# Performance work log

Measured on AMD Instinct MI355X. Metric: run time of the kernel, lower is better.

## Reference

```python
import jax, jax.numpy as jnp
import numpy as np

D_MODEL = 1024
N_HEAD = 16
D_FF = 4 * D_MODEL
LN_EPS = 1e-5


def _layernorm(x, g, b):
    mu = jnp.mean(x, axis=-1, keepdims=True)
    var = jnp.mean(jnp.square(x - mu), axis=-1, keepdims=True)
    return (x - mu) * jax.lax.rsqrt(var + LN_EPS) * g + b


def _mha(q_in, k_in, v_in, mask, wq, bq, wk, wv, bv, wo, bo):
    B, Tq, D = q_in.shape
    H, Dk = N_HEAD, D // N_HEAD
    q = (q_in @ wq + bq).reshape(B, Tq, H, Dk).transpose(0, 2, 1, 3)      # [B,H,Tq,Dk]
    k = (k_in @ wk).reshape(B, -1, H, Dk).transpose(0, 2, 1, 3)           # [B,H,Tk,Dk]
    v = (v_in @ wv + bv).reshape(B, -1, H, Dk).transpose(0, 2, 1, 3)      # [B,H,Tk,Dk]
    attn = jnp.einsum('bhqd,bhkd->bhqk', q, k) / jnp.sqrt(jnp.float32(Dk))
    if mask is not None:
        m0 = (mask[:, None, :, :] == 0)                                    # [B,1,Tq,Tk]
        attn = jnp.where(m0, -jnp.inf, attn)
        attn = jax.nn.softmax(attn, axis=-1)
        attn = jnp.where(m0, 0.0, attn)
    else:
        attn = jax.nn.softmax(attn, axis=-1)
    out = jnp.einsum('bhqk,bhkd->bhqd', attn, v)
    out = out.transpose(0, 2, 1, 3).reshape(B, Tq, D)
    return out @ wo + bo


def setup_inputs() -> dict:
    key = jax.random.key(0)
    ks = jax.random.split(key, 32)
    B, T, S, D = 4, 1024, 1024, D_MODEL
    w = lambda k, shp: 0.02 * jax.random.normal(k, shp, dtype=jnp.float32)
    inp = {
        'dec_input': jax.random.normal(ks[0], (B, T, D), dtype=jnp.float32),
        'enc_output': jax.random.normal(ks[1], (B, S, D), dtype=jnp.float32),
        'self_mask': jnp.broadcast_to(jnp.tril(jnp.ones((T, T), jnp.int32)), (B, T, T)),
        'cross_mask': jnp.ones((B, T, S), jnp.int32),
        'sa_ln_g': jnp.ones((D,), jnp.float32), 'sa_ln_b': jnp.zeros((D,), jnp.float32),
        'sa_wq': w(ks[2], (D, D)), 'sa_bq': jnp.zeros((D,), jnp.float32),
        'sa_wk': w(ks[3], (D, D)),
        'sa_wv': w(ks[4], (D, D)), 'sa_bv': jnp.zeros((D,), jnp.float32),
        'sa_wo': w(ks[5], (D, D)), 'sa_bo': jnp.zeros((D,), jnp.float32),
        'ca_ln_g': jnp.ones((D,), jnp.float32), 'ca_ln_b': jnp.zeros((D,), jnp.float32),
        'ca_wq': w(ks[6], (D, D)), 'ca_bq': jnp.zeros((D,), jnp.float32),
        'ca_wk': w(ks[7], (D, D)),
        'ca_wv': w(ks[8], (D, D)), 'ca_bv': jnp.zeros((D,), jnp.float32),
        'ca_wo': w(ks[9], (D, D)), 'ca_bo': jnp.zeros((D,), jnp.float32),
        'mlp_ln_g': jnp.ones((D,), jnp.float32), 'mlp_ln_b': jnp.zeros((D,), jnp.float32),
        'w1': w(ks[10], (D, D_FF)), 'b1': jnp.zeros((D_FF,), jnp.float32),
        'w2': w(ks[11], (D_FF, D)), 'b2': jnp.zeros((D,), jnp.float32),
    }
    return inp


def reference(dec_input, enc_output, self_mask, cross_mask,
              sa_ln_g, sa_ln_b, sa_wq, sa_bq, sa_wk, sa_wv, sa_bv, sa_wo, sa_bo,
              ca_ln_g, ca_ln_b, ca_wq, ca_bq, ca_wk, ca_wv, ca_bv, ca_wo, ca_bo,
              mlp_ln_g, mlp_ln_b, w1, b1, w2, b2):
    # self-attention block (pre-norm, residual)
    x = _layernorm(dec_input, sa_ln_g, sa_ln_b)
    x = dec_input + _mha(x, x, x, self_mask, sa_wq, sa_bq, sa_wk, sa_wv, sa_bv, sa_wo, sa_bo)
    # cross-attention block
    h = _layernorm(x, ca_ln_g, ca_ln_b)
    x = x + _mha(h, enc_output, enc_output, cross_mask, ca_wq, ca_bq, ca_wk, ca_wv, ca_bv, ca_wo, ca_bo)
    # GELU FFN block
    h = _layernorm(x, mlp_ln_g, mlp_ln_b)
    x = x + (jax.nn.gelu(h @ w1 + b1, approximate=False) @ w2 + b2)
    return x
```

## Files before the change

kernel.cpp:

```cpp
#include <hip/hip_runtime.h>
#include <math.h>

typedef unsigned short u16;
typedef unsigned int   u32;
typedef __attribute__((ext_vector_type(8))) short bf16x8;
typedef __attribute__((ext_vector_type(4))) float f32x4;

__device__ __forceinline__ u16 f2bf(float f) {
  u32 u = __builtin_bit_cast(u32, f);
  u += 0x7fffu + ((u >> 16) & 1u);
  return (u16)(u >> 16);
}
__device__ __forceinline__ u32 cvtpk(float lo, float hi_) {
  u32 r;
  asm("v_cvt_pk_bf16_f32 %0, %1, %2" : "=v"(r) : "v"(lo), "v"(hi_));
  return r;
}

__device__ __forceinline__ void g2l16(const u16* g, u16* l) {
  __builtin_amdgcn_global_load_lds(
      (const __attribute__((address_space(1))) unsigned int*)g,
      (__attribute__((address_space(3))) unsigned int*)l, 16, 0, 0);
}

struct TC8 { const float* s[8]; u16* d[8]; };
__global__ __launch_bounds__(256)
void transcvt8_kernel(TC8 p) {
  const float* __restrict__ W = p.s[blockIdx.z];
  u16* __restrict__ Wt = p.d[blockIdx.z];
  __shared__ float tile[32][33];
  const int n0 = blockIdx.x * 32, k0 = blockIdx.y * 32;
  const int tx = threadIdx.x & 31, ty = threadIdx.x >> 5;
  for (int i = 0; i < 4; ++i)
    tile[ty + 8 * i][tx] = W[(size_t)(k0 + ty + 8 * i) * 1024 + n0 + tx];
  __syncthreads();
  for (int i = 0; i < 4; ++i)
    Wt[(size_t)(n0 + ty + 8 * i) * 1024 + k0 + tx] = f2bf(tile[tx][ty + 8 * i]);
}

__global__ __launch_bounds__(256)
void transcvt_kernel(const float* __restrict__ W, u16* __restrict__ Wt, int K, int N) {
  __shared__ float tile[32][33];
  const int n0 = blockIdx.x * 32, k0 = blockIdx.y * 32;
  const int tx = threadIdx.x & 31, ty = threadIdx.x >> 5;
  for (int i = 0; i < 4; ++i)
    tile[ty + 8 * i][tx] = W[(size_t)(k0 + ty + 8 * i) * N + n0 + tx];
  __syncthreads();
  for (int i = 0; i < 4; ++i)
    Wt[(size_t)(n0 + ty + 8 * i) * K + k0 + tx] = f2bf(tile[tx][ty + 8 * i]);
}

__global__ __launch_bounds__(256)
void cvt_kernel(const float* __restrict__ in, u16* __restrict__ out) {
  const int i = blockIdx.x * 256 + threadIdx.x;
  const float4 v = ((const float4*)in)[i];
  u16 o[4] = {f2bf(v.x), f2bf(v.y), f2bf(v.z), f2bf(v.w)};
  ((ushort4*)out)[i] = *(ushort4*)o;
}

__global__ __launch_bounds__(256)
void pack_bias_kernel(const float* __restrict__ bq, const float* __restrict__ bv,
                      const float* __restrict__ cbv,
                      float* __restrict__ B3, float* __restrict__ B2) {
  const int i = blockIdx.x * 256 + threadIdx.x;
  if (i < 3072) {
    float v = 0.0f;
    if (i < 1024) v = bq[i];
    else if (i >= 2048) v = bv[i - 2048];
    B3[i] = v;
  } else {
    const int j = i - 3072;
    B2[j] = (j >= 1024) ? cbv[j - 1024] : 0.0f;
  }
}

__global__ __launch_bounds__(256)
void ln_kernel(const float* __restrict__ x, const float* __restrict__ g,
               const float* __restrict__ b, u16* __restrict__ out) {
  const int row = blockIdx.x;
  const float4 v4 = ((const float4*)(x + (size_t)row * 1024))[threadIdx.x];
  float vv[4] = {v4.x, v4.y, v4.z, v4.w};
  float s = vv[0] + vv[1] + vv[2] + vv[3];
  float s2 = vv[0] * vv[0] + vv[1] * vv[1] + vv[2] * vv[2] + vv[3] * vv[3];
  for (int m = 1; m < 64; m <<= 1) { s += __shfl_xor(s, m); s2 += __shfl_xor(s2, m); }
  __shared__ float ss[4], ss2[4];
  const int w = threadIdx.x >> 6;
  if ((threadIdx.x & 63) == 0) { ss[w] = s; ss2[w] = s2; }
  __syncthreads();
  s = ss[0] + ss[1] + ss[2] + ss[3];
  s2 = ss2[0] + ss2[1] + ss2[2] + ss2[3];
  const float mu = s * (1.0f / 1024.0f);
  const float var = s2 * (1.0f / 1024.0f) - mu * mu;
  const float r = rsqrtf(var + 1e-5f);
  const int c = threadIdx.x * 4;
  const float4 g4 = ((const float4*)g)[threadIdx.x];
  const float4 b4 = ((const float4*)b)[threadIdx.x];
  float gg[4] = {g4.x, g4.y, g4.z, g4.w};
  float bb[4] = {b4.x, b4.y, b4.z, b4.w};
  u16 o[4];
  for (int j = 0; j < 4; ++j) o[j] = f2bf((vv[j] - mu) * r * gg[j] + bb[j]);
  ((ushort4*)(out + (size_t)row * 1024 + c))[0] = *(ushort4*)o;
}

template<bool RES_F32, bool GELU>
__global__ __launch_bounds__(512)
void gemm_kernel(const u16* __restrict__ A, const u16* __restrict__ Bt,
                 const float* __restrict__ bias, const float* __restrict__ res,
                 void* __restrict__ Cout, int M, int N, int K) {
  __shared__ u16 As[2][128][32];
  __shared__ u16 Bs[2][128][32];
  const int t = threadIdx.x, lane = t & 63, w = t >> 6;
  const int wr = w >> 2, wc = w & 3;
  const int nwg = gridDim.x * gridDim.y;
  int bid = blockIdx.y * gridDim.x + blockIdx.x;
  bid = (bid & 7) * (nwg >> 3) + (bid >> 3);
  const int m0 = (bid / gridDim.x) * 128, n0 = (bid % gridDim.x) * 128;
  const int fr = lane & 15, fg = lane >> 4;
  const int srow = lane >> 2, scol = (lane & 3) * 8;
  const u16* Ag = &A[(size_t)(m0 + w * 16 + srow) * K + scol];
  const u16* Bg = &Bt[(size_t)(n0 + w * 16 + srow) * K + scol];
  f32x4 acc[4][2] = {};
  g2l16(Ag, &As[0][w * 16][0]);
  g2l16(Bg, &Bs[0][w * 16][0]);
  __syncthreads();
  int cur = 0;
  for (int k0 = 0; k0 < K; k0 += 32) {
    if (k0 + 32 < K) {
      const int nx = cur ^ 1, kn = k0 + 32;
      g2l16(Ag + kn, &As[nx][w * 16][0]);
      g2l16(Bg + kn, &Bs[nx][w * 16][0]);
    }
    bf16x8 af[4], bfr[2];
    for (int m = 0; m < 4; ++m) af[m] = *(bf16x8*)&As[cur][wr * 64 + m * 16 + fr][fg * 8];
    for (int n = 0; n < 2; ++n) bfr[n] = *(bf16x8*)&Bs[cur][wc * 32 + n * 16 + fr][fg * 8];
    __builtin_amdgcn_s_setprio(1);
    for (int m = 0; m < 4; ++m)
      for (int n = 0; n < 2; ++n)
        acc[m][n] = __builtin_amdgcn_mfma_f32_16x16x32_bf16(af[m], bfr[n], acc[m][n], 0, 0, 0);
    __builtin_amdgcn_s_setprio(0);
    __syncthreads();
    cur ^= 1;
  }
  for (int m = 0; m < 4; ++m)
    for (int n = 0; n < 2; ++n) {
      const int col = n0 + wc * 32 + n * 16 + fr;
      const float bv = bias ? bias[col] : 0.0f;
      for (int i = 0; i < 4; ++i) {
        const int row = m0 + wr * 64 + m * 16 + fg * 4 + i;
        float v = acc[m][n][i] + bv;
        if (GELU) v = 0.5f * v * (1.0f + erff(v * 0.70710678118654752f));
        if (RES_F32)
          ((float*)Cout)[(size_t)row * N + col] = res[(size_t)row * N + col] + v;
        else
          ((u16*)Cout)[(size_t)row * N + col] = f2bf(v);
      }
    }
}

template<bool CAUSAL>
__global__ __launch_bounds__(512)
void attn_kernel(const u16* __restrict__ Q, int ldq,
                 const u16* __restrict__ K, int ldk,
                 const u16* __restrict__ V, int ldv,
                 u16* __restrict__ O) {
  __shared__ u16 VsT[2][64][64];
  __shared__ u16 Ps[8][16][72];
  const int bh = blockIdx.x, b = bh >> 4, h = bh & 15;
  const int qy = blockIdx.y;
  const int t = threadIdx.x, w = t >> 6, lane = t & 63;
  const int ql = lane & 15;
  const int hi = lane >> 4;
  const int qr = qy * 128 + w * 16;
  const int qz = qr + ql;
  const int hcol = h * 64;
  const int nkt = CAUSAL ? 2 * qy + 2 : 16;
  const int wlim = CAUSAL ? (qr >> 6) : nkt - 1;
  const u16* Kb = K + (size_t)(b * 1024) * ldk + hcol;
  const u16* Vb = V + (size_t)(b * 1024) * ldv + hcol;
  const size_t qgrow = (size_t)(b * 1024 + qz) * ldq + hcol;
  const bf16x8 qb0 = *(const bf16x8*)&Q[qgrow + hi * 8];
  const bf16x8 qb1 = *(const bf16x8*)&Q[qgrow + 32 + hi * 8];
  f32x4 o[4] = {};
  float mrow = -1e30f, lsum = 0.0f;
  const int sp = t >> 3, sm = t & 7;
  const float c1 = 0.125f * 1.44269504f;
  if (t < 256) {
    const bf16x8 va = *(const bf16x8*)&Vb[(size_t)(2 * sp) * ldv + 8 * sm];
    const bf16x8 vb = *(const bf16x8*)&Vb[(size_t)(2 * sp + 1) * ldv + 8 * sm];
    #pragma unroll
    for (int jj = 0; jj < 8; ++jj) {
      u32 pr = (u32)((const u16*)&va)[jj] | ((u32)((const u16*)&vb)[jj] << 16);
      *(u32*)&VsT[0][8 * sm + jj][(2 * sp) ^ ((jj ^ sm) << 3)] = pr;
    }
  }
  bf16x8 kA[8], kB[8];
  #pragma unroll
  for (int j = 0; j < 4; ++j) {
    kA[j]     = *(const bf16x8*)&Kb[(size_t)(j * 16 + ql) * ldk + hi * 8];
    kA[4 + j] = *(const bf16x8*)&Kb[(size_t)(j * 16 + ql) * ldk + 32 + hi * 8];
  }
  __syncthreads();

  auto body = [&](bf16x8 (&kc)[8], bf16x8 (&kn)[8], const int kt) {
    const int k0 = kt * 64;
    bf16x8 va, vb;
    const bool stageV = (kt + 1 < nkt) && (t < 256);
    if (stageV) {
      va = *(const bf16x8*)&Vb[(size_t)(k0 + 64 + 2 * sp) * ldv + 8 * sm];
      vb = *(const bf16x8*)&Vb[(size_t)(k0 + 64 + 2 * sp + 1) * ldv + 8 * sm];
    }
    if (kt + 1 <= wlim) {
      #pragma unroll
      for (int j = 0; j < 4; ++j) {
        kn[j]     = *(const bf16x8*)&Kb[(size_t)(k0 + 64 + j * 16 + ql) * ldk + hi * 8];
        kn[4 + j] = *(const bf16x8*)&Kb[(size_t)(k0 + 64 + j * 16 + ql) * ldk + 32 + hi * 8];
      }
    }
    if (kt <= wlim) {
      f32x4 s[4] = {};
      __builtin_amdgcn_s_setprio(1);
      #pragma unroll
      for (int j = 0; j < 4; ++j)
        s[j] = __builtin_amdgcn_mfma_f32_16x16x32_bf16(kc[j], qb0, s[j], 0, 0, 0);
      #pragma unroll
      for (int j = 0; j < 4; ++j)
        s[j] = __builtin_amdgcn_mfma_f32_16x16x32_bf16(kc[4 + j], qb1, s[j], 0, 0, 0);
      __builtin_amdgcn_s_setprio(0);
      float e2[4][4];
      float rm = -1e30f;
      const bool domask = CAUSAL && (kt == wlim);
      #pragma unroll
      for (int j = 0; j < 4; ++j)
        #pragma unroll
        for (int i = 0; i < 4; ++i) {
          float a = s[j][i] * c1;
          if (domask && (k0 + j * 16 + hi * 4 + i > qz)) a = -1e30f;
          e2[j][i] = a;
          rm = fmaxf(rm, a);
        }
      if (!__all(rm <= mrow + 8.0f)) {
        rm = fmaxf(rm, __shfl_xor(rm, 16));
        rm = fmaxf(rm, __shfl_xor(rm, 32));
        const float mn = fmaxf(mrow, rm);
        const float sc = exp2f(mrow - mn);
        lsum *= sc;
        float scv[4];
        #pragma unroll
        for (int i = 0; i < 4; ++i) scv[i] = __shfl(sc, hi * 4 + i);
        #pragma unroll
        for (int nb = 0; nb < 4; ++nb)
          #pragma unroll
          for (int i = 0; i < 4; ++i) o[nb][i] *= scv[i];
        mrow = mn;
      }
      float p[4][4];
      #pragma unroll
      for (int j = 0; j < 4; ++j)
        #pragma unroll
        for (int i = 0; i < 4; ++i) { p[j][i] = exp2f(e2[j][i] - mrow); lsum += p[j][i]; }
      #pragma unroll
      for (int j = 0; j < 4; ++j) {
        *(u32*)&Ps[w][ql][j * 16 + hi * 4]     = cvtpk(p[j][0], p[j][1]);
        *(u32*)&Ps[w][ql][j * 16 + hi * 4 + 2] = cvtpk(p[j][2], p[j][3]);
      }
      asm volatile("s_waitcnt lgkmcnt(0)" ::: "memory");
      __builtin_amdgcn_sched_barrier(0);
      const bf16x8 pa0 = *(const bf16x8*)&Ps[w][ql][hi * 8];
      const bf16x8 pa1 = *(const bf16x8*)&Ps[w][ql][32 + hi * 8];
      __builtin_amdgcn_s_setprio(1);
      #pragma unroll
      for (int nb = 0; nb < 4; ++nb) {
        const int dim = nb * 16 + ql;
        const int swz = ((dim & 7) ^ ((dim >> 3) & 7)) << 3;
        const bf16x8 v0 = *(const bf16x8*)&VsT[kt & 1][dim][(hi * 8) ^ swz];
        const bf16x8 v1 = *(const bf16x8*)&VsT[kt & 1][dim][(32 + hi * 8) ^ swz];
        o[nb] = __builtin_amdgcn_mfma_f32_16x16x32_bf16(pa0, v0, o[nb], 0, 0, 0);
        o[nb] = __builtin_amdgcn_mfma_f32_16x16x32_bf16(pa1, v1, o[nb], 0, 0, 0);
      }
      __builtin_amdgcn_s_setprio(0);
    }
    if (stageV) {
      const int nx = (kt & 1) ^ 1;
      #pragma unroll
      for (int jj = 0; jj < 8; ++jj) {
        u32 pr = (u32)((const u16*)&va)[jj] | ((u32)((const u16*)&vb)[jj] << 16);
        *(u32*)&VsT[nx][8 * sm + jj][(2 * sp) ^ ((jj ^ sm) << 3)] = pr;
      }
    }
    __syncthreads();
  };

  for (int kt = 0; kt < nkt; kt += 2) {
    body(kA, kB, kt);
    if (kt + 1 < nkt) body(kB, kA, kt + 1);
  }

  float ltot = lsum + __shfl_xor(lsum, 16);
  ltot += __shfl_xor(ltot, 32);
  const float inv = 1.0f / ltot;
  #pragma unroll
  for (int i = 0; i < 4; ++i) {
    const float invq = __shfl(inv, hi * 4 + i);
    const size_t row = (size_t)(b * 1024 + qr + hi * 4 + i);
    #pragma unroll
    for (int nb = 0; nb < 4; ++nb)
      O[row * 1024 + hcol + nb * 16 + ql] = f2bf(o[nb][i] * invq);
  }
}

extern "C" void kernel_launch(void* const* d_in, const int* in_sizes, int n_in,
                              void* d_out, int out_size, void* d_ws, size_t ws_size,
                              hipStream_t stream) {
  const float* dec  = (const float*)d_in[0];
  const float* enc  = (const float*)d_in[1];
  const float* sa_g = (const float*)d_in[4];
  const float* sa_b = (const float*)d_in[5];
  const float* sa_wq = (const float*)d_in[6];
  const float* sa_bq = (const float*)d_in[7];
  const float* sa_wk = (const float*)d_in[8];
  const float* sa_wv = (const float*)d_in[9];
  const float* sa_bv = (const float*)d_in[10];
  const float* sa_wo = (const float*)d_in[11];
  const float* sa_bo = (const float*)d_in[12];
  const float* ca_g = (const float*)d_in[13];
  const float* ca_b = (const float*)d_in[14];
  const float* ca_wq = (const float*)d_in[15];
  const float* ca_bq = (const float*)d_in[16];
  const float* ca_wk = (const float*)d_in[17];
  const float* ca_wv = (const float*)d_in[18];
  const float* ca_bv = (const float*)d_in[19];
  const float* ca_wo = (const float*)d_in[20];
  const float* ca_bo = (const float*)d_in[21];
  const float* mlp_g = (const float*)d_in[22];
  const float* mlp_b = (const float*)d_in[23];
  const float* w1 = (const float*)d_in[24];
  const float* b1 = (const float*)d_in[25];
  const float* w2 = (const float*)d_in[26];
  const float* b2 = (const float*)d_in[27];

  const size_t MB = 1024 * 1024;
  if (ws_size < 97 * MB) return;
  char* ws = (char*)d_ws;
  u16* WQKV = (u16*)(ws + 0 * MB);
  u16* CQT  = (u16*)(ws + 6 * MB);
  u16* CKV  = (u16*)(ws + 8 * MB);
  u16* WOT  = (u16*)(ws + 12 * MB);
  u16* COT  = (u16*)(ws + 14 * MB);
  float* B3 = (float*)(ws + 16 * MB);
  float* B2 = (float*)(ws + 16 * MB + 16384);
  u16* XLN  = (u16*)(ws + 17 * MB);
  u16* AO   = (u16*)(ws + 25 * MB);
  u16* W1T  = (u16*)(ws + 25 * MB);
  u16* ENC  = (u16*)(ws + 33 * MB);
  u16* FB   = (u16*)(ws + 41 * MB);
  u16* EF   = (u16*)(ws + 41 * MB);
  u16* CQB  = (u16*)(ws + 57 * MB);
  u16* H1   = (u16*)(ws + 33 * MB);
  float* X1 = (float*)(ws + 65 * MB);
  u16* W2T  = (u16*)(ws + 65 * MB);
  float* X2 = (float*)(ws + 81 * MB);
  float* OUT = (float*)d_out;

  const dim3 blk(256), gblk(512), ablk(512);
  TC8 tc;
  tc.s[0] = sa_wq; tc.d[0] = WQKV;
  tc.s[1] = sa_wk; tc.d[1] = WQKV + 1024 * 1024;
  tc.s[2] = sa_wv; tc.d[2] = WQKV + 2048 * 1024;
  tc.s[3] = sa_wo; tc.d[3] = WOT;
  tc.s[4] = ca_wq; tc.d[4] = CQT;
  tc.s[5] = ca_wk; tc.d[5] = CKV;
  tc.s[6] = ca_wv; tc.d[6] = CKV + 1024 * 1024;
  tc.s[7] = ca_wo; tc.d[7] = COT;
  transcvt8_kernel<<<dim3(32, 32, 8), blk, 0, stream>>>(tc);
  pack_bias_kernel<<<dim3(20), blk, 0, stream>>>(sa_bq, sa_bv, ca_bv, B3, B2);
  cvt_kernel<<<dim3(4096), blk, 0, stream>>>(enc, ENC);

  ln_kernel<<<dim3(4096), blk, 0, stream>>>(dec, sa_g, sa_b, XLN);
  gemm_kernel<false, false><<<dim3(24, 32), gblk, 0, stream>>>(XLN, WQKV, B3, nullptr, FB, 4096, 3072, 1024);
  attn_kernel<true><<<dim3(64, 8), ablk, 0, stream>>>(FB, 3072, FB + 1024, 3072, FB + 2048, 3072, AO);
  gemm_kernel<true, false><<<dim3(8, 32), gblk, 0, stream>>>(AO, WOT, sa_bo, dec, X1, 4096, 1024, 1024);

  ln_kernel<<<dim3(4096), blk, 0, stream>>>(X1, ca_g, ca_b, XLN);
  gemm_kernel<false, false><<<dim3(16, 32), gblk, 0, stream>>>(ENC, CKV, B2, nullptr, EF, 4096, 2048, 1024);
  gemm_kernel<false, false><<<dim3(8, 32), gblk, 0, stream>>>(XLN, CQT, ca_bq, nullptr, CQB, 4096, 1024, 1024);
  attn_kernel<false><<<dim3(64, 8), ablk, 0, stream>>>(CQB, 1024, EF, 2048, EF + 1024, 2048, AO);
  gemm_kernel<true, false><<<dim3(8, 32), gblk, 0, stream>>>(AO, COT, ca_bo, X1, X2, 4096, 1024, 1024);

  transcvt_kernel<<<dim3(128, 32), blk, 0, stream>>>(w1, W1T, 1024, 4096);
  transcvt_kernel<<<dim3(32, 128), blk, 0, stream>>>(w2, W2T, 4096, 1024);
  ln_kernel<<<dim3(4096), blk, 0, stream>>>(X2, mlp_g, mlp_b, XLN);
  gemm_kernel<false, true><<<dim3(32, 32), gblk, 0, stream>>>(XLN, W1T, b1, nullptr, H1, 4096, 4096, 1024);
  gemm_kernel<true, false><<<dim3(8, 32), gblk, 0, stream>>>(H1, W2T, b2, X2, OUT, 4096, 1024, 4096);
}
```

Measured before the change: 451.5 us.

## Pre-transpose V in a separate kernel and keep attention P in registers

Adds a vtrans kernel that writes V as a per-head transposed buffer, so attention reads V fragments directly from global memory instead of staging them through a swizzled LDS double buffer. The P matrix is rearranged into MFMA operand layout with cross-lane shuffles instead of a round trip through shared memory. This removes all LDS use and __syncthreads from the attention loop. Attention blocks shrink to 256 threads covering 64 query rows, doubling the grid. The trade is two extra kernel launches, an extra V write and read through global memory, and more shuffle instructions per tile.

```diff
diff --git a/kernel.cpp b/kernel.cpp
--- a/kernel.cpp
+++ b/kernel.cpp
@@ -5,6 +5,7 @@
 typedef unsigned int   u32;
 typedef __attribute__((ext_vector_type(8))) short bf16x8;
 typedef __attribute__((ext_vector_type(4))) float f32x4;
+typedef __attribute__((ext_vector_type(4))) u32 u32x4;
 
 __device__ __forceinline__ u16 f2bf(float f) {
   u32 u = __builtin_bit_cast(u32, f);
@@ -48,6 +49,25 @@
   __syncthreads();
   for (int i = 0; i < 4; ++i)
     Wt[(size_t)(n0 + ty + 8 * i) * K + k0 + tx] = f2bf(tile[tx][ty + 8 * i]);
+}
+
+__global__ __launch_bounds__(256)
+void vtrans_kernel(const u16* __restrict__ V, int ldv, u16* __restrict__ VT) {
+  __shared__ u16 tile[64][72];
+  const int bh = blockIdx.y, b = bh >> 4, h = bh & 15;
+  const int k0 = blockIdx.x * 64;
+  const int t = threadIdx.x;
+  const int r = t >> 2, c16 = (t & 3) * 16;
+  const u16* src = &V[(size_t)(b * 1024 + k0 + r) * ldv + h * 64 + c16];
+  *(bf16x8*)&tile[r][c16] = *(const bf16x8*)&src[0];
+  *(bf16x8*)&tile[r][c16 + 8] = *(const bf16x8*)&src[8];
+  __syncthreads();
+  u16 tmp[16];
+  #pragma unroll
+  for (int j = 0; j < 16; ++j) tmp[j] = tile[c16 + j][r];
+  u16* dst = &VT[((size_t)bh << 16) + (size_t)r * 1024 + k0 + c16];
+  *(bf16x8*)&dst[0] = *(bf16x8*)&tmp[0];
+  *(bf16x8*)&dst[8] = *(bf16x8*)&tmp[8];
 }
 
 __global__ __launch_bounds__(256)
@@ -158,136 +178,128 @@
 }
 
 template<bool CAUSAL>
-__global__ __launch_bounds__(512)
+__global__ __launch_bounds__(256)
 void attn_kernel(const u16* __restrict__ Q, int ldq,
                  const u16* __restrict__ K, int ldk,
-                 const u16* __restrict__ V, int ldv,
+                 const u16* __restrict__ VT,
                  u16* __restrict__ O) {
-  __shared__ u16 VsT[2][64][64];
-  __shared__ u16 Ps[8][16][72];
   const int bh = blockIdx.x, b = bh >> 4, h = bh & 15;
   const int qy = blockIdx.y;
   const int t = threadIdx.x, w = t >> 6, lane = t & 63;
   const int ql = lane & 15;
   const int hi = lane >> 4;
-  const int qr = qy * 128 + w * 16;
+  const int qr = qy * 64 + w * 16;
   const int qz = qr + ql;
   const int hcol = h * 64;
-  const int nkt = CAUSAL ? 2 * qy + 2 : 16;
-  const int wlim = CAUSAL ? (qr >> 6) : nkt - 1;
+  const int nkt = CAUSAL ? qy + 1 : 16;
   const u16* Kb = K + (size_t)(b * 1024) * ldk + hcol;
-  const u16* Vb = V + (size_t)(b * 1024) * ldv + hcol;
+  const u16* Vb = VT + ((size_t)bh << 16);
   const size_t qgrow = (size_t)(b * 1024 + qz) * ldq + hcol;
   const bf16x8 qb0 = *(const bf16x8*)&Q[qgrow + hi * 8];
   const bf16x8 qb1 = *(const bf16x8*)&Q[qgrow + 32 + hi * 8];
   f32x4 o[4] = {};
   float mrow = -1e30f, lsum = 0.0f;
-  const int sp = t >> 3, sm = t & 7;
   const float c1 = 0.125f * 1.44269504f;
-  if (t < 256) {
-    const bf16x8 va = *(const bf16x8*)&Vb[(size_t)(2 * sp) * ldv + 8 * sm];
-    const bf16x8 vb = *(const bf16x8*)&Vb[(size_t)(2 * sp + 1) * ldv + 8 * sm];
-    #pragma unroll
-    for (int jj = 0; jj < 8; ++jj) {
-      u32 pr = (u32)((const u16*)&va)[jj] | ((u32)((const u16*)&vb)[jj] << 16);
-      *(u32*)&VsT[0][8 * sm + jj][(2 * sp) ^ ((jj ^ sm) << 3)] = pr;
-    }
-  }
+  const bool odd = (lane & 16) != 0;
+
   bf16x8 kA[8], kB[8];
   #pragma unroll
   for (int j = 0; j < 4; ++j) {
     kA[j]     = *(const bf16x8*)&Kb[(size_t)(j * 16 + ql) * ldk + hi * 8];
     kA[4 + j] = *(const bf16x8*)&Kb[(size_t)(j * 16 + ql) * ldk + 32 + hi * 8];
   }
-  __syncthreads();
 
   auto body = [&](bf16x8 (&kc)[8], bf16x8 (&kn)[8], const int kt) {
     const int k0 = kt * 64;
-    bf16x8 va, vb;
-    const bool stageV = (kt + 1 < nkt) && (t < 256);
-    if (stageV) {
-      va = *(const bf16x8*)&Vb[(size_t)(k0 + 64 + 2 * sp) * ldv + 8 * sm];
-      vb = *(const bf16x8*)&Vb[(size_t)(k0 + 64 + 2 * sp + 1) * ldv + 8 * sm];
-    }
-    if (kt + 1 <= wlim) {
+    bf16x8 vf[4][2];
+    #pragma unroll
+    for (int nb = 0; nb < 4; ++nb) {
+      const u16* vrow = &Vb[(size_t)(nb * 16 + ql) * 1024 + k0];
+      vf[nb][0] = *(const bf16x8*)&vrow[hi * 8];
+      vf[nb][1] = *(const bf16x8*)&vrow[32 + hi * 8];
+    }
+    if (kt + 1 < nkt) {
       #pragma unroll
       for (int j = 0; j < 4; ++j) {
         kn[j]     = *(const bf16x8*)&Kb[(size_t)(k0 + 64 + j * 16 + ql) * ldk + hi * 8];
         kn[4 + j] = *(const bf16x8*)&Kb[(size_t)(k0 + 64 + j * 16 + ql) * ldk + 32 + hi * 8];
       }
     }
-    if (kt <= wlim) {
-      f32x4 s[4] = {};
-      __builtin_amdgcn_s_setprio(1);
+    f32x4 s[4] = {};
+    __builtin_amdgcn_s_setprio(1);
+    #pragma unroll
+    for (int j = 0; j < 4; ++j)
+      s[j] = __builtin_amdgcn_mfma_f32_16x16x32_bf16(kc[j], qb0, s[j], 0, 0, 0);
+    #pragma unroll
+    for (int j = 0; j < 4; ++j)
+      s[j] = __builtin_amdgcn_mfma_f32_16x16x32_bf16(kc[4 + j], qb1, s[j], 0, 0, 0);
+    __builtin_amdgcn_s_setprio(0);
+    float e2[4][4];
+    float rm = -1e30f;
+    const bool domask = CAUSAL && (kt == nkt - 1);
+    #pragma unroll
+    for (int j = 0; j < 4; ++j)
       #pragma unroll
-      for (int j = 0; j < 4; ++j)
-        s[j] = __builtin_amdgcn_mfma_f32_16x16x32_bf16(kc[j], qb0, s[j], 0, 0, 0);
+      for (int i = 0; i < 4; ++i) {
+        float a = s[j][i] * c1;
+        if (domask && (k0 + j * 16 + hi * 4 + i > qz)) a = -1e30f;
+        e2[j][i] = a;
+        rm = fmaxf(rm, a);
+      }
+    if (!__all(rm <= mrow + 8.0f)) {
+      rm = fmaxf(rm, __shfl_xor(rm, 16));
+      rm = fmaxf(rm, __shfl_xor(rm, 32));
+      const float mn = fmaxf(mrow, rm);
+      const float sc = exp2f(mrow - mn);
+      lsum *= sc;
+      float scv[4];
       #pragma unroll
-      for (int j = 0; j < 4; ++j)
-        s[j] = __builtin_amdgcn_mfma_f32_16x16x32_bf16(kc[4 + j], qb1, s[j], 0, 0, 0);
-      __builtin_amdgcn_s_setprio(0);
-      float e2[4][4];
-      float rm = -1e30f;
-      const bool domask = CAUSAL && (kt == wlim);
+      for (int i = 0; i < 4; ++i) scv[i] = __shfl(sc, hi * 4 + i);
       #pragma unroll
-      for (int j = 0; j < 4; ++j)
+      for (int nb = 0; nb < 4; ++nb)
         #pragma unroll
-        for (int i = 0; i < 4; ++i) {
-          float a = s[j][i] * c1;
-          if (domask && (k0 + j * 16 + hi * 4 + i > qz)) a = -1e30f;
-          e2[j][i] = a;
-          rm = fmaxf(rm, a);
-        }
-      if (!__all(rm <= mrow + 8.0f)) {
-        rm = fmaxf(rm, __shfl_xor(rm, 16));
-        rm = fmaxf(rm, __shfl_xor(rm, 32));
-        const float mn = fmaxf(mrow, rm);
-        const float sc = exp2f(mrow - mn);
-        lsum *= sc;
-        float scv[4];
-        #pragma unroll
-        for (int i = 0; i < 4; ++i) scv[i] = __shfl(sc, hi * 4 + i);
-        #pragma unroll
-        for (int nb = 0; nb < 4; ++nb)
-          #pragma unroll
-          for (int i = 0; i < 4; ++i) o[nb][i] *= scv[i];
-        mrow = mn;
-      }
-      float p[4][4];
+        for (int i = 0; i < 4; ++i) o[nb][i] *= scv[i];
+      mrow = mn;
+    }
+    float p[4][4];
+    #pragma unroll
+    for (int j = 0; j < 4; ++j)
       #pragma unroll
-      for (int j = 0; j < 4; ++j)
-        #pragma unroll
-        for (int i = 0; i < 4; ++i) { p[j][i] = exp2f(e2[j][i] - mrow); lsum += p[j][i]; }
-      #pragma unroll
-      for (int j = 0; j < 4; ++j) {
-        *(u32*)&Ps[w][ql][j * 16 + hi * 4]     = cvtpk(p[j][0], p[j][1]);
-        *(u32*)&Ps[w][ql][j * 16 + hi * 4 + 2] = cvtpk(p[j][2], p[j][3]);
-      }
-      asm volatile("s_waitcnt lgkmcnt(0)" ::: "memory");
-      __builtin_amdgcn_sched_barrier(0);
-      const bf16x8 pa0 = *(const bf16x8*)&Ps[w][ql][hi * 8];
-      const bf16x8 pa1 = *(const bf16x8*)&Ps[w][ql][32 + hi * 8];
-      __builtin_amdgcn_s_setprio(1);
-      #pragma unroll
-      for (int nb = 0; nb < 4; ++nb) {
-        const int dim = nb * 16 + ql;
-        const int swz = ((dim & 7) ^ ((dim >> 3) & 7)) << 3;
-        const bf16x8 v0 = *(const bf16x8*)&VsT[kt & 1][dim][(hi * 8) ^ swz];
-        const bf16x8 v1 = *(const bf16x8*)&VsT[kt & 1][dim][(32 + hi * 8) ^ swz];
-        o[nb] = __builtin_amdgcn_mfma_f32_16x16x32_bf16(pa0, v0, o[nb], 0, 0, 0);
-        o[nb] = __builtin_amdgcn_mfma_f32_16x16x32_bf16(pa1, v1, o[nb], 0, 0, 0);
-      }
-      __builtin_amdgcn_s_setprio(0);
-    }
-    if (stageV) {
-      const int nx = (kt & 1) ^ 1;
-      #pragma unroll
-      for (int jj = 0; jj < 8; ++jj) {
-        u32 pr = (u32)((const u16*)&va)[jj] | ((u32)((const u16*)&vb)[jj] << 16);
-        *(u32*)&VsT[nx][8 * sm + jj][(2 * sp) ^ ((jj ^ sm) << 3)] = pr;
-      }
-    }
-    __syncthreads();
+      for (int i = 0; i < 4; ++i) { p[j][i] = exp2f(e2[j][i] - mrow); lsum += p[j][i]; }
+    u32 Wd0[4], Wd1[4];
+    #pragma unroll
+    for (int j = 0; j < 4; ++j) {
+      Wd0[j] = cvtpk(p[j][0], p[j][1]);
+      Wd1[j] = cvtpk(p[j][2], p[j][3]);
+    }
+    bf16x8 pa[2];
+    #pragma unroll
+    for (int m = 0; m < 2; ++m) {
+      u32 a0 = Wd0[2 * m], b0 = Wd0[2 * m + 1];
+      u32 a1 = Wd1[2 * m], b1 = Wd1[2 * m + 1];
+      const u32 sa0 = __shfl_xor((int)a0, 32), sb0 = __shfl_xor((int)b0, 32);
+      const u32 sa1 = __shfl_xor((int)a1, 32), sb1 = __shfl_xor((int)b1, 32);
+      const bool lo32 = lane < 32;
+      const u32 A0 = lo32 ? a0 : sb0, B0 = lo32 ? sa0 : b0;
+      const u32 A1 = lo32 ? a1 : sb1, B1 = lo32 ? sa1 : b1;
+      const u32 P0 = odd ? A0 : B0, S0 = odd ? B0 : A0;
+      const u32 P1 = odd ? A1 : B1, S1 = odd ? B1 : A1;
+      const u32 X0 = __shfl_xor((int)P0, 16);
+      const u32 X1 = __shfl_xor((int)P1, 16);
+      u32x4 wv;
+      wv.x = odd ? X0 : S0;
+      wv.y = odd ? X1 : S1;
+      wv.z = odd ? S0 : X0;
+      wv.w = odd ? S1 : X1;
+      pa[m] = __builtin_bit_cast(bf16x8, wv);
+    }
+    __builtin_amdgcn_s_setprio(1);
+    #pragma unroll
+    for (int nb = 0; nb < 4; ++nb) {
+      o[nb] = __builtin_amdgcn_mfma_f32_16x16x32_bf16(pa[0], vf[nb][0], o[nb], 0, 0, 0);
+      o[nb] = __builtin_amdgcn_mfma_f32_16x16x32_bf16(pa[1], vf[nb][1], o[nb], 0, 0, 0);
+    }
+    __builtin_amdgcn_s_setprio(0);
   };
 
   for (int kt = 0; kt < nkt; kt += 2) {
@@ -357,11 +369,13 @@
   u16* CQB  = (u16*)(ws + 57 * MB);
   u16* H1   = (u16*)(ws + 33 * MB);
   float* X1 = (float*)(ws + 65 * MB);
+  u16* VTs  = (u16*)(ws + 65 * MB);
   u16* W2T  = (u16*)(ws + 65 * MB);
+  u16* VTc  = (u16*)(ws + 17 * MB);
   float* X2 = (float*)(ws + 81 * MB);
   float* OUT = (float*)d_out;
 
-  const dim3 blk(256), gblk(512), ablk(512);
+  const dim3 blk(256), gblk(512);
   TC8 tc;
   tc.s[0] = sa_wq; tc.d[0] = WQKV;
   tc.s[1] = sa_wk; tc.d[1] = WQKV + 1024 * 1024;
@@ -377,13 +391,15 @@
 
   ln_kernel<<<dim3(4096), blk, 0, stream>>>(dec, sa_g, sa_b, XLN);
   gemm_kernel<false, false><<<dim3(24, 32), gblk, 0, stream>>>(XLN, WQKV, B3, nullptr, FB, 4096, 3072, 1024);
-  attn_kernel<true><<<dim3(64, 8), ablk, 0, stream>>>(FB, 3072, FB + 1024, 3072, FB + 2048, 3072, AO);
+  vtrans_kernel<<<dim3(16, 64), blk, 0, stream>>>(FB + 2048, 3072, VTs);
+  attn_kernel<true><<<dim3(64, 16), blk, 0, stream>>>(FB, 3072, FB + 1024, 3072, VTs, AO);
   gemm_kernel<true, false><<<dim3(8, 32), gblk, 0, stream>>>(AO, WOT, sa_bo, dec, X1, 4096, 1024, 1024);
 
   ln_kernel<<<dim3(4096), blk, 0, stream>>>(X1, ca_g, ca_b, XLN);
   gemm_kernel<false, false><<<dim3(16, 32), gblk, 0, stream>>>(ENC, CKV, B2, nullptr, EF, 4096, 2048, 1024);
   gemm_kernel<false, false><<<dim3(8, 32), gblk, 0, stream>>>(XLN, CQT, ca_bq, nullptr, CQB, 4096, 1024, 1024);
-  attn_kernel<false><<<dim3(64, 8), ablk, 0, stream>>>(CQB, 1024, EF, 2048, EF + 1024, 2048, AO);
+  vtrans_kernel<<<dim3(16, 64), blk, 0, stream>>>(EF + 1024, 2048, VTc);
+  attn_kernel<false><<<dim3(64, 16), blk, 0, stream>>>(CQB, 1024, EF, 2048, VTc, AO);
   gemm_kernel<true, false><<<dim3(8, 32), gblk, 0, stream>>>(AO, COT, ca_bo, X1, X2, 4096, 1024, 1024);
 
   transcvt_kernel<<<dim3(128, 32), blk, 0, stream>>>(w1, W1T, 1024, 4096);
```

Result: slower. 506.2 us (+12.1%).
